# Performance work log

Hardware: AMD Instinct MI355X
Metric: run time of the kernel (lower is better)

Reference implementation:

```python
import jax, jax.numpy as jnp
import numpy as np

B, S, H, NH = 2, 2048, 1024, 16
HD = H // NH
SCALE = float(H) ** 0.5  # note: source scales by sqrt(hidden_dim), not sqrt(head_dim)
EPS = 1e-5


def setup_inputs() -> dict:
    key = jax.random.key(0)
    ks = jax.random.split(key, 16)
    s = 0.02
    return {
        "q": jax.random.normal(ks[0], (B, S, H), jnp.float32),
        "k": jax.random.normal(ks[1], (B, S, H), jnp.float32),
        "v": jax.random.normal(ks[2], (B, S, H), jnp.float32),
        "mask": jax.random.randint(ks[3], (B, 1, S, S), 0, 2, jnp.int32),
        "Wq": jax.random.normal(ks[4], (H, H), jnp.float32) * s,
        "bq": jnp.zeros((H,), jnp.float32),
        "Wk": jax.random.normal(ks[5], (H, H), jnp.float32) * s,
        "bk": jnp.zeros((H,), jnp.float32),
        "Wv": jax.random.normal(ks[6], (H, H), jnp.float32) * s,
        "bv": jnp.zeros((H,), jnp.float32),
        "Wfc": jax.random.normal(ks[7], (H, H), jnp.float32) * s,
        "bfc": jnp.zeros((H,), jnp.float32),
        "gamma": jnp.ones((H,), jnp.float32),
        "beta": jnp.zeros((H,), jnp.float32),
    }


def reference(q, k, v, mask, Wq, bq, Wk, bk, Wv, bv, Wfc, bfc, gamma, beta):
    residual = q
    qh = (q @ Wq + bq).reshape(B, S, NH, HD)
    kh = (k @ Wk + bk).reshape(B, S, NH, HD)
    vh = (v @ Wv + bv).reshape(B, S, NH, HD)
    # full [B, NH, S, S] score matrix, as in the source
    energy = jnp.einsum('nqhd,nkhd->nhqk', qh, kh)
    energy = jnp.where(mask == 0, jnp.float32(-1e9), energy)
    attn = jax.nn.softmax(energy / SCALE, axis=3)  # dropout p=0.0 -> identity
    out = jnp.einsum('nhqk,nkhd->nqhd', attn, vh).reshape(B, S, H)
    y = out @ Wfc + bfc + residual
    mu = jnp.mean(y, axis=-1, keepdims=True)
    var = jnp.mean((y - mu) ** 2, axis=-1, keepdims=True)
    return gamma * (y - mu) / jnp.sqrt(var + EPS) + beta
```

## Files before the change

### kernel.cpp

```cpp
#include <hip/hip_runtime.h>
#include <hip/hip_bf16.h>

#define S_LEN  2048
#define HDIM   1024
#define NHEADS 16
#define HEADD  64
#define BATCH  2
#define MTOT   (BATCH * S_LEN)
#define K2EXP  0.04508422f

typedef __attribute__((ext_vector_type(8)))  __bf16 bf16x8;
typedef __attribute__((ext_vector_type(4)))  __bf16 bf16x4;
typedef __attribute__((ext_vector_type(4)))  float  f32x4;
typedef __attribute__((ext_vector_type(16))) float  f32x16;

__device__ __forceinline__ void gload16(const void* g, void* l) {
  __builtin_amdgcn_global_load_lds(
      (const __attribute__((address_space(1))) void*)g,
      (__attribute__((address_space(3))) void*)l, 16, 0, 0);
}
template<int STRIDE>
__device__ __forceinline__ bf16x8 lds_rdS(const __bf16* base, int row, int bcol) {
  const char* p = (const char*)base + row * STRIDE + (bcol ^ ((row & (STRIDE / 16 - 1)) << 4));
  return *(const bf16x8*)p;
}
__device__ __forceinline__ unsigned cvtpk_bf16(float lo, float hi) {
  unsigned r;
  asm("v_cvt_pk_bf16_f32 %0, %1, %2" : "=v"(r) : "v"(lo), "v"(hi));
  return r;
}
__device__ __forceinline__ void plswap(unsigned& a, unsigned& b) {
  asm volatile("v_permlane32_swap_b32 %0, %1" : "+v"(a), "+v"(b));
}

__global__ __launch_bounds__(256)
void prologue_kernel(const float* __restrict__ q, const float* __restrict__ k,
                     const float* __restrict__ v, const int* __restrict__ mask,
                     const float* __restrict__ Wq, const float* __restrict__ Wk,
                     const float* __restrict__ Wv, const float* __restrict__ Wfc,
                     __bf16* __restrict__ Qc, __bf16* __restrict__ Kc,
                     __bf16* __restrict__ Vc, unsigned* __restrict__ mbH,
                     __bf16* __restrict__ Wt)
{
  __shared__ float T[64][65];
  const int id = blockIdx.x;
  const int tid = threadIdx.x;
  if (id < 6144) {
    const int z = id >> 11, blk = id & 2047;
    const float* src = (z == 0) ? q : (z == 1) ? k : v;
    __bf16* dst = (z == 0) ? Qc : (z == 1) ? Kc : Vc;
    const size_t i = ((size_t)blk * 256 + tid) * 8;
    const float4 a = *(const float4*)&src[i];
    const float4 c = *(const float4*)&src[i + 4];
    bf16x8 o;
    o[0] = (__bf16)a.x; o[1] = (__bf16)a.y; o[2] = (__bf16)a.z; o[3] = (__bf16)a.w;
    o[4] = (__bf16)c.x; o[5] = (__bf16)c.y; o[6] = (__bf16)c.z; o[7] = (__bf16)c.w;
    *(bf16x8*)&dst[i] = o;
  } else if (id < 38912) {
    const size_t idx = (size_t)(id - 6144) * 256 + tid;
    const int m = mask[idx];
    const unsigned long long bal = __ballot(m != 0);
    const int lane = tid & 63;
    if ((lane & 31) == 0) {
      const int hh = lane >> 5;
      unsigned wlo = 0, whi = 0;
      #pragma unroll
      for (int j = 0; j < 16; ++j) {
        const int kvl = (j & 3) + 8 * (j >> 2) + 4 * hh;
        wlo |= (unsigned)((bal >> kvl) & 1ULL) << j;
        whi |= (unsigned)((bal >> (32 + kvl)) & 1ULL) << j;
      }
      const int b   = (int)(idx >> 22);
      const int qq  = (int)(idx >> 11) & 2047;
      const int seg = ((int)idx & 2047) >> 6;
      mbH[(((size_t)(hh * 2 + b)) * 32 + seg) * S_LEN + qq] = wlo | (whi << 16);
    }
  } else {
    const int f = id - 38912;
    const int z = f >> 8;
    const float* W = (z == 0) ? Wq : (z == 1) ? Wk : (z == 2) ? Wv : Wfc;
    const float sc = (z == 0) ? K2EXP : 1.0f;
    __bf16* O = Wt + (size_t)z * HDIM * HDIM;
    const int k0 = ((f >> 4) & 15) * 64, n0 = (f & 15) * 64;
    const int r  = tid >> 4;
    const int c4 = (tid & 15) * 4;
    #pragma unroll
    for (int p = 0; p < 4; ++p) {
      const int row = r + p * 16;
      const float4 vv = *(const float4*)&W[(size_t)(k0 + row) * HDIM + n0 + c4];
      T[row][c4 + 0] = vv.x; T[row][c4 + 1] = vv.y;
      T[row][c4 + 2] = vv.z; T[row][c4 + 3] = vv.w;
    }
    __syncthreads();
    #pragma unroll
    for (int p = 0; p < 4; ++p) {
      const int n = r + p * 16;
      bf16x4 o;
      #pragma unroll
      for (int i = 0; i < 4; ++i) o[i] = (__bf16)(T[c4 + i][n] * sc);
      *(bf16x4*)&O[(size_t)(n0 + n) * HDIM + k0 + c4] = o;
    }
  }
}

template<int MODE, int BMT>
__device__ __forceinline__ void gemm_body(
    __bf16* As, __bf16* Bs,
    const __bf16* __restrict__ A, const __bf16* __restrict__ Wt,
    const float* __restrict__ bias, float bscale,
    const float* __restrict__ resid,
    __bf16* __restrict__ Ob, float* __restrict__ Of, __bf16* __restrict__ Vtg)
{
  constexpr int AI = BMT / 32;
  const int tid = threadIdx.x, lane = tid & 63, w = tid >> 6;
  const int fr = lane & 15, k8 = (lane >> 4) * 8;
  const int wr = w >> 1, wc = w & 1;
  const int f   = blockIdx.x + gridDim.x * blockIdx.y;
  const int cpx = (gridDim.x * gridDim.y) >> 3;
  const int fs  = (f & 7) * cpx + (f >> 3);
  const int m0 = (fs / gridDim.x) * BMT, n0 = (fs % gridDim.x) * 128;
  const int srow8 = lane >> 3, slot = lane & 7;

  f32x4 acc[AI][4] = {};

  #define G_STAGE(kt, bf)                                                    \
    {                                                                        \
      _Pragma("unroll")                                                      \
      for (int c = 0; c < AI; ++c) {                                         \
        const int ra = w * (BMT / 4) + c * 8 + srow8;                        \
        gload16(&A[(size_t)(m0 + ra) * HDIM + (kt) * 64 + ((slot ^ (ra & 7)) * 8)], \
                (void*)&As[((bf) * BMT + ra) * 64]);                         \
      }                                                                      \
      _Pragma("unroll")                                                      \
      for (int c = 0; c < 4; ++c) {                                          \
        const int rb = w * 32 + c * 8 + srow8;                               \
        gload16(&Wt[(size_t)(n0 + rb) * HDIM + (kt) * 64 + ((slot ^ (rb & 7)) * 8)], \
                (void*)&Bs[((bf) * 128 + rb) * 64]);                         \
      }                                                                      \
    }

  #define G_COMPUTE(bf)                                                      \
    {                                                                        \
      _Pragma("unroll")                                                      \
      for (int kk = 0; kk < 64; kk += 32) {                                  \
        bf16x8 a[AI], b[4];                                                  \
        _Pragma("unroll")                                                    \
        for (int i = 0; i < AI; ++i)                                         \
          a[i] = lds_rdS<128>(&As[(bf) * BMT * 64], wr * (BMT / 2) + i * 16 + fr, (kk + k8) * 2); \
        _Pragma("unroll")                                                    \
        for (int j = 0; j < 4; ++j)                                          \
          b[j] = lds_rdS<128>(&Bs[(bf) * 128 * 64], wc * 64 + j * 16 + fr, (kk + k8) * 2); \
        _Pragma("unroll")                                                    \
        for (int i = 0; i < AI; ++i)                                         \
          _Pragma("unroll")                                                  \
          for (int j = 0; j < 4; ++j)                                        \
            acc[i][j] = __builtin_amdgcn_mfma_f32_16x16x32_bf16(a[i], b[j], acc[i][j], 0, 0, 0); \
      }                                                                      \
    }

  G_STAGE(0, 0)
  for (int kt = 0; kt < 15; ++kt) {
    G_STAGE(kt + 1, (kt + 1) & 1)
    if constexpr (BMT == 128) asm volatile("s_waitcnt vmcnt(8)" ::: "memory");
    else                      asm volatile("s_waitcnt vmcnt(6)" ::: "memory");
    __builtin_amdgcn_s_barrier();
    __builtin_amdgcn_sched_barrier(0);
    __builtin_amdgcn_s_setprio(1);
    G_COMPUTE(kt & 1)
    __builtin_amdgcn_s_setprio(0);
    __builtin_amdgcn_sched_barrier(0);
    __builtin_amdgcn_s_barrier();
  }
  asm volatile("s_waitcnt vmcnt(0)" ::: "memory");
  __builtin_amdgcn_s_barrier();
  G_COMPUTE(1)

  const int rg = (lane >> 4) * 4;
  #pragma unroll
  for (int i = 0; i < AI; ++i) {
    #pragma unroll
    for (int j = 0; j < 4; ++j) {
      const int col = n0 + wc * 64 + j * 16 + fr;
      if constexpr (MODE == 2) {
        const int h = col >> 6, hd = col & 63;
        const int row = m0 + wr * (BMT / 2) + i * 16 + rg;
        const int bq = row >> 11, qq = row & 2047;
        bf16x4 o;
        #pragma unroll
        for (int r = 0; r < 4; ++r) o[r] = (__bf16)(acc[i][j][r] + bias[col]);
        *(bf16x4*)&Vtg[(((size_t)bq * NHEADS + h) * HEADD + hd) * S_LEN + qq] = o;
      } else {
        #pragma unroll
        for (int r = 0; r < 4; ++r) {
          const int row = m0 + wr * (BMT / 2) + i * 16 + rg + r;
          if constexpr (MODE == 0) {
            Ob[(size_t)row * HDIM + col] = (__bf16)(acc[i][j][r] + bias[col] * bscale);
          } else {
            Of[(size_t)row * HDIM + col] =
                acc[i][j][r] + bias[col] + resid[(size_t)row * HDIM + col];
          }
        }
      }
    }
  }
  #undef G_STAGE
  #undef G_COMPUTE
}

__global__ __launch_bounds__(256)
void qkv_kernel(const __bf16* __restrict__ Qc, const __bf16* __restrict__ Kc,
                const __bf16* __restrict__ Vc, const __bf16* __restrict__ Wt,
                const float* __restrict__ bq, const float* __restrict__ bk,
                const float* __restrict__ bv,
                __bf16* __restrict__ Qb, __bf16* __restrict__ Kb,
                __bf16* __restrict__ Vtg)
{
  __shared__ __bf16 smem[2 * 128 * 64 * 2];
  __bf16* As = smem;
  __bf16* Bs = smem + 2 * 128 * 64;
  const int z = blockIdx.z;
  if (z == 2) {
    gemm_body<2, 128>(As, Bs, Vc, Wt + (size_t)2 * HDIM * HDIM, bv, 1.0f,
                      nullptr, nullptr, nullptr, Vtg);
  } else {
    gemm_body<0, 128>(As, Bs, z ? Kc : Qc, Wt + (size_t)z * HDIM * HDIM,
                      z ? bk : bq, z ? 1.0f : K2EXP, nullptr,
                      z ? Kb : Qb, nullptr, nullptr);
  }
}

__global__ __launch_bounds__(256)
void fc_kernel(const __bf16* __restrict__ A, const __bf16* __restrict__ Wt,
               const float* __restrict__ bias, const float* __restrict__ resid,
               float* __restrict__ Of)
{
  __shared__ __bf16 smem[2 * 64 * 64 + 2 * 128 * 64];
  __bf16* As = smem;
  __bf16* Bs = smem + 2 * 64 * 64;
  gemm_body<1, 64>(As, Bs, A, Wt + (size_t)3 * HDIM * HDIM, bias, 1.0f, resid,
                   nullptr, Of, nullptr);
}

__global__ __launch_bounds__(256)
void attn_kernel(const __bf16* __restrict__ Qb, const __bf16* __restrict__ Kb,
                 const __bf16* __restrict__ Vtg, const unsigned* __restrict__ mbH,
                 __bf16* __restrict__ AO)
{
  __shared__ __bf16 Ks[2][64][64];
  __shared__ __bf16 Vt[2][64][64];

  const int bh = blockIdx.x, b = bh >> 4, h = bh & 15;
  const int tid = threadIdx.x, lane = tid & 63, w = tid >> 6;
  const int fr = lane & 31, hi = lane >> 5;
  const int qw = blockIdx.y * 128 + w * 32;
  const int q  = qw + fr;

  bf16x8 qf[4];
  #pragma unroll
  for (int st = 0; st < 4; ++st)
    qf[st] = *(const bf16x8*)&Qb[((size_t)b * S_LEN + q) * HDIM + h * HEADD + st * 16 + hi * 8];

  const int srl = w * 16 + (lane >> 3);
  const int ssw = ((lane & 7) ^ (srl & 7)) * 8;
  const __bf16* ksrc = Kb  + ((size_t)b * S_LEN + srl) * HDIM + h * HEADD + ssw;
  const __bf16* vsrc = Vtg + ((size_t)bh * HEADD + srl) * S_LEN + ssw;
  const unsigned* tbl = mbH + ((size_t)(hi * 2 + b) * 32) * S_LEN + q;

  bf16x8 ones;
  #pragma unroll
  for (int e = 0; e < 8; ++e) ones[e] = (__bf16)1.0f;

  f32x16 o0 = {}, o1 = {}, l_acc = {};
  unsigned mv, nm = 0;

  mv = tbl[0];
  gload16(ksrc,             (void*)&Ks[0][w * 16][0]);
  gload16(ksrc + 8 * HDIM,  (void*)&Ks[0][w * 16 + 8][0]);
  gload16(vsrc,             (void*)&Vt[0][w * 16][0]);
  gload16(vsrc + 8 * S_LEN, (void*)&Vt[0][w * 16 + 8][0]);

  for (int t = 0; t < 32; ++t) {
    const int buf = t & 1;
    __builtin_amdgcn_s_barrier();
    if (t < 31) {
      nm = tbl[(size_t)(t + 1) * S_LEN];
      const __bf16* kp = ksrc + (size_t)(t + 1) * 64 * HDIM;
      const __bf16* vp = vsrc + (size_t)(t + 1) * 64;
      gload16(kp,             (void*)&Ks[buf ^ 1][w * 16][0]);
      gload16(kp + 8 * HDIM,  (void*)&Ks[buf ^ 1][w * 16 + 8][0]);
      gload16(vp,             (void*)&Vt[buf ^ 1][w * 16][0]);
      gload16(vp + 8 * S_LEN, (void*)&Vt[buf ^ 1][w * 16 + 8][0]);
      asm volatile("s_waitcnt vmcnt(5)" ::: "memory");
    } else {
      asm volatile("s_waitcnt vmcnt(0)" ::: "memory");
    }
    __builtin_amdgcn_sched_barrier(0);

    const __bf16* Kbuf = &Ks[buf][0][0];
    const __bf16* Vbuf = &Vt[buf][0][0];

    f32x16 s0 = {}, s1 = {};
    __builtin_amdgcn_s_setprio(1);
    #pragma unroll
    for (int st = 0; st < 4; ++st) {
      s0 = __builtin_amdgcn_mfma_f32_32x32x16_bf16(
          lds_rdS<128>(Kbuf, fr,      st * 32 + hi * 16), qf[st], s0, 0, 0, 0);
      s1 = __builtin_amdgcn_mfma_f32_32x32x16_bf16(
          lds_rdS<128>(Kbuf, 32 + fr, st * 32 + hi * 16), qf[st], s1, 0, 0, 0);
    }
    __builtin_amdgcn_s_setprio(0);

    {
      float pp[16];
      #pragma unroll
      for (int j = 0; j < 16; ++j) {
        const float e0 = __builtin_amdgcn_exp2f(s0[j]);
        const unsigned a0 = (unsigned)__builtin_amdgcn_sbfe(mv, j, 1);
        pp[j] = __uint_as_float(a0 & __float_as_uint(e0));
      }
      bf16x8 pa[2];
      #pragma unroll
      for (int g = 0; g < 2; ++g) {
        const int o = g * 8;
        unsigned x  = cvtpk_bf16(pp[o + 0], pp[o + 1]);
        unsigned x2 = cvtpk_bf16(pp[o + 2], pp[o + 3]);
        unsigned y  = cvtpk_bf16(pp[o + 4], pp[o + 5]);
        unsigned y2 = cvtpk_bf16(pp[o + 6], pp[o + 7]);
        plswap(x, y);
        plswap(x2, y2);
        union { unsigned u[4]; bf16x8 v; } uu;
        uu.u[0] = x; uu.u[1] = x2; uu.u[2] = y; uu.u[3] = y2;
        pa[g] = uu.v;
      }
      __builtin_amdgcn_s_setprio(1);
      #pragma unroll
      for (int g = 0; g < 2; ++g) {
        l_acc = __builtin_amdgcn_mfma_f32_32x32x16_bf16(pa[g], ones, l_acc, 0, 0, 0);
        o0 = __builtin_amdgcn_mfma_f32_32x32x16_bf16(
            pa[g], lds_rdS<128>(Vbuf, fr,      g * 32 + hi * 16), o0, 0, 0, 0);
        o1 = __builtin_amdgcn_mfma_f32_32x32x16_bf16(
            pa[g], lds_rdS<128>(Vbuf, 32 + fr, g * 32 + hi * 16), o1, 0, 0, 0);
      }
      __builtin_amdgcn_s_setprio(0);
    }

    {
      float pp[16];
      #pragma unroll
      for (int j = 0; j < 16; ++j) {
        const float e1 = __builtin_amdgcn_exp2f(s1[j]);
        const unsigned a1 = (unsigned)__builtin_amdgcn_sbfe(mv, j + 16, 1);
        pp[j] = __uint_as_float(a1 & __float_as_uint(e1));
      }
      bf16x8 pa[2];
      #pragma unroll
      for (int g = 0; g < 2; ++g) {
        const int o = g * 8;
        unsigned x  = cvtpk_bf16(pp[o + 0], pp[o + 1]);
        unsigned x2 = cvtpk_bf16(pp[o + 2], pp[o + 3]);
        unsigned y  = cvtpk_bf16(pp[o + 4], pp[o + 5]);
        unsigned y2 = cvtpk_bf16(pp[o + 6], pp[o + 7]);
        plswap(x, y);
        plswap(x2, y2);
        union { unsigned u[4]; bf16x8 v; } uu;
        uu.u[0] = x; uu.u[1] = x2; uu.u[2] = y; uu.u[3] = y2;
        pa[g] = uu.v;
      }
      __builtin_amdgcn_s_setprio(1);
      #pragma unroll
      for (int g = 0; g < 2; ++g) {
        l_acc = __builtin_amdgcn_mfma_f32_32x32x16_bf16(pa[g], ones, l_acc, 0, 0, 0);
        o0 = __builtin_amdgcn_mfma_f32_32x32x16_bf16(
            pa[g], lds_rdS<128>(Vbuf, fr,      (2 + g) * 32 + hi * 16), o0, 0, 0, 0);
        o1 = __builtin_amdgcn_mfma_f32_32x32x16_bf16(
            pa[g], lds_rdS<128>(Vbuf, 32 + fr, (2 + g) * 32 + hi * 16), o1, 0, 0, 0);
      }
      __builtin_amdgcn_s_setprio(0);
    }

    mv = nm;
  }

  #pragma unroll
  for (int g = 0; g < 4; ++g) {
    #pragma unroll
    for (int r = 0; r < 4; ++r) {
      const int j = g * 4 + r;
      const float inv = __builtin_amdgcn_rcpf(l_acc[j]);
      const int qq = qw + g * 8 + hi * 4 + r;
      AO[((size_t)b * S_LEN + qq) * HDIM + h * HEADD + fr]      = (__bf16)(o0[j] * inv);
      AO[((size_t)b * S_LEN + qq) * HDIM + h * HEADD + 32 + fr] = (__bf16)(o1[j] * inv);
    }
  }
}

__global__ __launch_bounds__(256)
void ln_kernel(float* __restrict__ y, const float* __restrict__ gamma,
               const float* __restrict__ beta)
{
  __shared__ float red[8];
  const int tid = threadIdx.x;
  float* p = y + (size_t)blockIdx.x * HDIM;

  float4 vv = *(const float4*)&p[tid * 4];
  float s  = vv.x + vv.y + vv.z + vv.w;
  float ss = vv.x * vv.x + vv.y * vv.y + vv.z * vv.z + vv.w * vv.w;
  #pragma unroll
  for (int d = 1; d < 64; d <<= 1) {
    s  += __shfl_xor(s, d);
    ss += __shfl_xor(ss, d);
  }
  const int wid = tid >> 6;
  if ((tid & 63) == 0) { red[wid * 2] = s; red[wid * 2 + 1] = ss; }
  __syncthreads();
  s  = red[0] + red[2] + red[4] + red[6];
  ss = red[1] + red[3] + red[5] + red[7];
  const float mean = s * (1.0f / HDIM);
  const float var  = ss * (1.0f / HDIM) - mean * mean;
  const float inv  = rsqrtf(var + 1e-5f);

  const float4 g  = *(const float4*)&gamma[tid * 4];
  const float4 bt = *(const float4*)&beta[tid * 4];
  vv.x = (vv.x - mean) * inv * g.x + bt.x;
  vv.y = (vv.y - mean) * inv * g.y + bt.y;
  vv.z = (vv.z - mean) * inv * g.z + bt.z;
  vv.w = (vv.w - mean) * inv * g.w + bt.w;
  *(float4*)&p[tid * 4] = vv;
}

extern "C" void kernel_launch(void* const* d_in, const int* in_sizes, int n_in,
                              void* d_out, int out_size, void* d_ws, size_t ws_size,
                              hipStream_t stream) {
  const float* q     = (const float*)d_in[0];
  const float* k     = (const float*)d_in[1];
  const float* v     = (const float*)d_in[2];
  const int*   mask  = (const int*)  d_in[3];
  const float* Wq    = (const float*)d_in[4];
  const float* bq    = (const float*)d_in[5];
  const float* Wk    = (const float*)d_in[6];
  const float* bk    = (const float*)d_in[7];
  const float* Wv    = (const float*)d_in[8];
  const float* bv    = (const float*)d_in[9];
  const float* Wfc   = (const float*)d_in[10];
  const float* bfc   = (const float*)d_in[11];
  const float* gamma = (const float*)d_in[12];
  const float* beta  = (const float*)d_in[13];
  float* out = (float*)d_out;

  char* ws = (char*)d_ws;
  const size_t MB16 = (size_t)MTOT * HDIM * 2;
  unsigned* mbH = (unsigned*)ws;
  __bf16* Wt  = (__bf16*)(ws + (1u << 20));
  __bf16* Qc  = (__bf16*)(ws + (1u << 20) + 4 * (size_t)HDIM * HDIM * 2);
  __bf16* Kc  = (__bf16*)((char*)Qc + MB16);
  __bf16* Vc  = (__bf16*)((char*)Kc + MB16);
  __bf16* Qb  = (__bf16*)((char*)Vc + MB16);
  __bf16* Kb  = (__bf16*)((char*)Qb + MB16);
  __bf16* Vtg = (__bf16*)((char*)Kb + MB16);
  __bf16* AO  = Kc;

  const dim3 blk(256);

  prologue_kernel<<<dim3(39936), blk, 0, stream>>>(
      q, k, v, mask, Wq, Wk, Wv, Wfc, Qc, Kc, Vc, mbH, Wt);

  qkv_kernel<<<dim3(HDIM / 128, MTOT / 128, 3), blk, 0, stream>>>(
      Qc, Kc, Vc, Wt, bq, bk, bv, Qb, Kb, Vtg);

  attn_kernel<<<dim3(BATCH * NHEADS, S_LEN / 128), blk, 0, stream>>>(
      Qb, Kb, Vtg, mbH, AO);

  fc_kernel<<<dim3(HDIM / 128, MTOT / 64), blk, 0, stream>>>(
      AO, Wt, bfc, q, out);

  ln_kernel<<<dim3(MTOT), blk, 0, stream>>>(out, gamma, beta);
}
```

Baseline: 160.5 us.

## Split each KV tile across wave pairs in attention and merge partials via LDS

The attention kernel now gives each 32-query slab to two waves, each handling half of every 64-key tile. The block covers 64 queries instead of 128, so the grid doubles. At the end, one wave writes its partial O and row-sum accumulators to shared memory and the other adds them before normalizing. This is meant to raise parallelism and occupancy and to shorten per-wave dependency chains. In exchange, K/V tiles are loaded twice as often across the grid, and a final LDS reduction with extra barriers is added.

```diff
diff --git a/kernel.cpp b/kernel.cpp
--- a/kernel.cpp
+++ b/kernel.cpp
@@ -246,13 +246,15 @@
                  const __bf16* __restrict__ Vtg, const unsigned* __restrict__ mbH,
                  __bf16* __restrict__ AO)
 {
-  __shared__ __bf16 Ks[2][64][64];
-  __shared__ __bf16 Vt[2][64][64];
+  __shared__ __align__(16) char smem[32768];
+  __bf16 (*Ks)[64][64] = (__bf16(*)[64][64])smem;
+  __bf16 (*Vt)[64][64] = (__bf16(*)[64][64])(smem + 16384);
 
   const int bh = blockIdx.x, b = bh >> 4, h = bh & 15;
   const int tid = threadIdx.x, lane = tid & 63, w = tid >> 6;
   const int fr = lane & 31, hi = lane >> 5;
-  const int qw = blockIdx.y * 128 + w * 32;
+  const int qt = w >> 1, kvh = w & 1;
+  const int qw = blockIdx.y * 64 + qt * 32;
   const int q  = qw + fr;
 
   bf16x8 qf[4];
@@ -299,97 +301,74 @@
     const __bf16* Kbuf = &Ks[buf][0][0];
     const __bf16* Vbuf = &Vt[buf][0][0];
 
-    f32x16 s0 = {}, s1 = {};
+    f32x16 s = {};
     __builtin_amdgcn_s_setprio(1);
     #pragma unroll
-    for (int st = 0; st < 4; ++st) {
-      s0 = __builtin_amdgcn_mfma_f32_32x32x16_bf16(
-          lds_rdS<128>(Kbuf, fr,      st * 32 + hi * 16), qf[st], s0, 0, 0, 0);
-      s1 = __builtin_amdgcn_mfma_f32_32x32x16_bf16(
-          lds_rdS<128>(Kbuf, 32 + fr, st * 32 + hi * 16), qf[st], s1, 0, 0, 0);
-    }
+    for (int st = 0; st < 4; ++st)
+      s = __builtin_amdgcn_mfma_f32_32x32x16_bf16(
+          lds_rdS<128>(Kbuf, kvh * 32 + fr, st * 32 + hi * 16), qf[st], s, 0, 0, 0);
     __builtin_amdgcn_s_setprio(0);
 
-    {
-      float pp[16];
+    float pp[16];
+    #pragma unroll
+    for (int j = 0; j < 16; ++j) {
+      const float e = __builtin_amdgcn_exp2f(s[j]);
+      const unsigned a = (unsigned)__builtin_amdgcn_sbfe(mv, j + 16 * kvh, 1);
+      pp[j] = __uint_as_float(a & __float_as_uint(e));
+    }
+
+    bf16x8 pa[2];
+    #pragma unroll
+    for (int g = 0; g < 2; ++g) {
+      const int o = g * 8;
+      unsigned x  = cvtpk_bf16(pp[o + 0], pp[o + 1]);
+      unsigned x2 = cvtpk_bf16(pp[o + 2], pp[o + 3]);
+      unsigned y  = cvtpk_bf16(pp[o + 4], pp[o + 5]);
+      unsigned y2 = cvtpk_bf16(pp[o + 6], pp[o + 7]);
+      plswap(x, y);
+      plswap(x2, y2);
+      union { unsigned u[4]; bf16x8 v; } uu;
+      uu.u[0] = x; uu.u[1] = x2; uu.u[2] = y; uu.u[3] = y2;
+      pa[g] = uu.v;
+    }
+
+    __builtin_amdgcn_s_setprio(1);
+    #pragma unroll
+    for (int g = 0; g < 2; ++g) {
+      const int bcol = kvh * 64 + g * 32 + hi * 16;
+      l_acc = __builtin_amdgcn_mfma_f32_32x32x16_bf16(pa[g], ones, l_acc, 0, 0, 0);
+      o0 = __builtin_amdgcn_mfma_f32_32x32x16_bf16(
+          pa[g], lds_rdS<128>(Vbuf, fr,      bcol), o0, 0, 0, 0);
+      o1 = __builtin_amdgcn_mfma_f32_32x32x16_bf16(
+          pa[g], lds_rdS<128>(Vbuf, 32 + fr, bcol), o1, 0, 0, 0);
+    }
+    __builtin_amdgcn_s_setprio(0);
+
+    mv = nm;
+  }
+
+  __builtin_amdgcn_s_barrier();
+  float* sh = (float*)smem;
+  if (kvh) {
+    float* p = sh + ((size_t)qt * 64 + lane) * 48;
+    #pragma unroll
+    for (int j = 0; j < 16; ++j) { p[j] = o0[j]; p[16 + j] = o1[j]; p[32 + j] = l_acc[j]; }
+  }
+  __builtin_amdgcn_s_barrier();
+  if (!kvh) {
+    const float* p = sh + ((size_t)qt * 64 + lane) * 48;
+    #pragma unroll
+    for (int g = 0; g < 4; ++g) {
       #pragma unroll
-      for (int j = 0; j < 16; ++j) {
-        const float e0 = __builtin_amdgcn_exp2f(s0[j]);
-        const unsigned a0 = (unsigned)__builtin_amdgcn_sbfe(mv, j, 1);
-        pp[j] = __uint_as_float(a0 & __float_as_uint(e0));
+      for (int r = 0; r < 4; ++r) {
+        const int j = g * 4 + r;
+        const float inv = __builtin_amdgcn_rcpf(l_acc[j] + p[32 + j]);
+        const int qq = qw + g * 8 + hi * 4 + r;
+        AO[((size_t)b * S_LEN + qq) * HDIM + h * HEADD + fr]      =
+            (__bf16)((o0[j] + p[j]) * inv);
+        AO[((size_t)b * S_LEN + qq) * HDIM + h * HEADD + 32 + fr] =
+            (__bf16)((o1[j] + p[16 + j]) * inv);
       }
-      bf16x8 pa[2];
-      #pragma unroll
-      for (int g = 0; g < 2; ++g) {
-        const int o = g * 8;
-        unsigned x  = cvtpk_bf16(pp[o + 0], pp[o + 1]);
-        unsigned x2 = cvtpk_bf16(pp[o + 2], pp[o + 3]);
-        unsigned y  = cvtpk_bf16(pp[o + 4], pp[o + 5]);
-        unsigned y2 = cvtpk_bf16(pp[o + 6], pp[o + 7]);
-        plswap(x, y);
-        plswap(x2, y2);
-        union { unsigned u[4]; bf16x8 v; } uu;
-        uu.u[0] = x; uu.u[1] = x2; uu.u[2] = y; uu.u[3] = y2;
-        pa[g] = uu.v;
-      }
-      __builtin_amdgcn_s_setprio(1);
-      #pragma unroll
-      for (int g = 0; g < 2; ++g) {
-        l_acc = __builtin_amdgcn_mfma_f32_32x32x16_bf16(pa[g], ones, l_acc, 0, 0, 0);
-        o0 = __builtin_amdgcn_mfma_f32_32x32x16_bf16(
-            pa[g], lds_rdS<128>(Vbuf, fr,      g * 32 + hi * 16), o0, 0, 0, 0);
-        o1 = __builtin_amdgcn_mfma_f32_32x32x16_bf16(
-            pa[g], lds_rdS<128>(Vbuf, 32 + fr, g * 32 + hi * 16), o1, 0, 0, 0);
-      }
-      __builtin_amdgcn_s_setprio(0);
-    }
-
-    {
-      float pp[16];
-      #pragma unroll
-      for (int j = 0; j < 16; ++j) {
-        const float e1 = __builtin_amdgcn_exp2f(s1[j]);
-        const unsigned a1 = (unsigned)__builtin_amdgcn_sbfe(mv, j + 16, 1);
-        pp[j] = __uint_as_float(a1 & __float_as_uint(e1));
-      }
-      bf16x8 pa[2];
-      #pragma unroll
-      for (int g = 0; g < 2; ++g) {
-        const int o = g * 8;
-        unsigned x  = cvtpk_bf16(pp[o + 0], pp[o + 1]);
-        unsigned x2 = cvtpk_bf16(pp[o + 2], pp[o + 3]);
-        unsigned y  = cvtpk_bf16(pp[o + 4], pp[o + 5]);
-        unsigned y2 = cvtpk_bf16(pp[o + 6], pp[o + 7]);
-        plswap(x, y);
-        plswap(x2, y2);
-        union { unsigned u[4]; bf16x8 v; } uu;
-        uu.u[0] = x; uu.u[1] = x2; uu.u[2] = y; uu.u[3] = y2;
-        pa[g] = uu.v;
-      }
-      __builtin_amdgcn_s_setprio(1);
-      #pragma unroll
-      for (int g = 0; g < 2; ++g) {
-        l_acc = __builtin_amdgcn_mfma_f32_32x32x16_bf16(pa[g], ones, l_acc, 0, 0, 0);
-        o0 = __builtin_amdgcn_mfma_f32_32x32x16_bf16(
-            pa[g], lds_rdS<128>(Vbuf, fr,      (2 + g) * 32 + hi * 16), o0, 0, 0, 0);
-        o1 = __builtin_amdgcn_mfma_f32_32x32x16_bf16(
-            pa[g], lds_rdS<128>(Vbuf, 32 + fr, (2 + g) * 32 + hi * 16), o1, 0, 0, 0);
-      }
-      __builtin_amdgcn_s_setprio(0);
-    }
-
-    mv = nm;
-  }
-
-  #pragma unroll
-  for (int g = 0; g < 4; ++g) {
-    #pragma unroll
-    for (int r = 0; r < 4; ++r) {
-      const int j = g * 4 + r;
-      const float inv = __builtin_amdgcn_rcpf(l_acc[j]);
-      const int qq = qw + g * 8 + hi * 4 + r;
-      AO[((size_t)b * S_LEN + qq) * HDIM + h * HEADD + fr]      = (__bf16)(o0[j] * inv);
-      AO[((size_t)b * S_LEN + qq) * HDIM + h * HEADD + 32 + fr] = (__bf16)(o1[j] * inv);
     }
   }
 }
@@ -467,7 +446,7 @@
   qkv_kernel<<<dim3(HDIM / 128, MTOT / 128, 3), blk, 0, stream>>>(
       Qc, Kc, Vc, Wt, bq, bk, bv, Qb, Kb, Vtg);
 
-  attn_kernel<<<dim3(BATCH * NHEADS, S_LEN / 128), blk, 0, stream>>>(
+  attn_kernel<<<dim3(BATCH * NHEADS, S_LEN / 64), blk, 0, stream>>>(
       Qb, Kb, Vtg, mbH, AO);
 
   fc_kernel<<<dim3(HDIM / 128, MTOT / 64), blk, 0, stream>>>(
```

New measurement: 169.3 us. 5.5% more time.
